# Kernel optimization log

Measured on AMD Instinct MI355X. Metric: run time of the kernel, lower is better.

Reference implementation:

```python
import jax, jax.numpy as jnp
import numpy as np

B, L, H, A = 512, 256, 512, 128
IENC, VDIM, EDIM, CDIM = 512, 512, 512, 512


def _lstm_cell(x, h, c, w_ih, w_hh, b_ih, b_hh):
    # PyTorch LSTMCell: gates ordered (i, f, g, o)
    gates = x @ w_ih.T + h @ w_hh.T + b_ih + b_hh
    i, f, g, o = jnp.split(gates, 4, axis=1)
    c_new = jax.nn.sigmoid(f) * c + jax.nn.sigmoid(i) * jnp.tanh(g)
    h_new = jax.nn.sigmoid(o) * jnp.tanh(c_new)
    return h_new, c_new


def setup_inputs() -> dict:
    key = jax.random.key(0)
    ks = jax.random.split(key, 32)
    s = 0.02  # param init scale
    d = {
        'xt': jax.random.normal(ks[0], (B, IENC), jnp.float32),
        'video': jax.random.normal(ks[1], (VDIM,), jnp.float32),
        'event': jax.random.normal(ks[2], (B, EDIM), jnp.float32),
        'clip': jax.random.normal(ks[3], (B, L, CDIM), jnp.float32),
        'clip_mask': jax.random.randint(ks[4], (B, L), 0, 2, jnp.int32),
        'state_h': jax.random.normal(ks[5], (3, B, H), jnp.float32),
        'state_c': jax.random.normal(ks[6], (3, B, H), jnp.float32),
        # layer0: in = VDIM + H + IENC
        'w_ih0': jax.random.normal(ks[7], (4 * H, VDIM + H + IENC), jnp.float32) * s,
        'w_hh0': jax.random.normal(ks[8], (4 * H, H), jnp.float32) * s,
        'b_ih0': jnp.zeros((4 * H,), jnp.float32),
        'b_hh0': jnp.zeros((4 * H,), jnp.float32),
        # layer1: in = EDIM + H
        'w_ih1': jax.random.normal(ks[9], (4 * H, EDIM + H), jnp.float32) * s,
        'w_hh1': jax.random.normal(ks[10], (4 * H, H), jnp.float32) * s,
        'b_ih1': jnp.zeros((4 * H,), jnp.float32),
        'b_hh1': jnp.zeros((4 * H,), jnp.float32),
        # layer2: in = CDIM + H
        'w_ih2': jax.random.normal(ks[11], (4 * H, CDIM + H), jnp.float32) * s,
        'w_hh2': jax.random.normal(ks[12], (4 * H, H), jnp.float32) * s,
        'b_ih2': jnp.zeros((4 * H,), jnp.float32),
        'b_hh2': jnp.zeros((4 * H,), jnp.float32),
        # attention params
        'wc': jax.random.normal(ks[13], (A, CDIM), jnp.float32) * s,
        'bc': jnp.zeros((A,), jnp.float32),
        'wh': jax.random.normal(ks[14], (A, H), jnp.float32) * s,
        'bh': jnp.zeros((A,), jnp.float32),
        'wa': jax.random.normal(ks[15], (1, A), jnp.float32) * s,
        'ba': jnp.zeros((1,), jnp.float32),
    }
    return d


def reference(xt, video, event, clip, clip_mask, state_h, state_c,
              w_ih0, w_hh0, b_ih0, b_hh0,
              w_ih1, w_hh1, b_ih1, b_hh1,
              w_ih2, w_hh2, b_ih2, b_hh2,
              wc, bc, wh, bh, wa, ba):
    pre_h = state_h[-1]                                   # [B,H]
    video_b = jnp.broadcast_to(video[None, :], (xt.shape[0], video.shape[0]))
    # layer 0 (dropout is identity in eval mode)
    x0 = jnp.concatenate([xt, video_b, pre_h], axis=1)
    h0, c0 = _lstm_cell(x0, state_h[0], state_c[0], w_ih0, w_hh0, b_ih0, b_hh0)
    # layer 1
    x1 = jnp.concatenate([event, h0], axis=1)
    h1, c1 = _lstm_cell(x1, state_h[1], state_c[1], w_ih1, w_hh1, b_ih1, b_hh1)
    # Bahdanau additive attention over clip tokens
    att = jnp.einsum('blc,ac->bla', clip, wc) + bc        # [B,L,A]
    att_h = h1 @ wh.T + bh                                # [B,A]
    dot = jnp.tanh(att + att_h[:, None, :])               # [B,L,A]
    scores = jnp.einsum('bla,a->bl', dot, wa[0]) + ba[0]  # [B,L]
    weight = jax.nn.softmax(scores, axis=1)
    m = clip_mask.astype(weight.dtype)
    weight = weight * m
    weight = weight / jnp.sum(weight, axis=1, keepdims=True)
    att_res = jnp.einsum('bl,blc->bc', weight, clip)      # [B,CDIM]
    # layer 2
    x2 = jnp.concatenate([att_res, h1], axis=1)
    h2, c2 = _lstm_cell(x2, state_h[2], state_c[2], w_ih2, w_hh2, b_ih2, b_hh2)
    new_h = jnp.stack([h0, h1, h2])
    new_c = jnp.stack([c0, c1, c2])
    return h2, new_h, new_c
```

## Files before the change

### kernel.cpp

```cpp
#include <hip/hip_runtime.h>
#include <math.h>

typedef __attribute__((ext_vector_type(8))) short bf16x8;
typedef __attribute__((ext_vector_type(4))) float f32x4;

constexpr int LST = 72;
constexpr int AST = 520;

__device__ __forceinline__ unsigned short f2b(float f) {
    union { float f; unsigned int i; } c; c.f = f;
    unsigned int i = c.i;
    return (unsigned short)((i + 0x7fffu + ((i >> 16) & 1u)) >> 16);
}
__device__ __forceinline__ void unpack2(unsigned int v, float& lo, float& hi) {
    union { unsigned int i; float f; } c0, c1;
    c0.i = v << 16; c1.i = v & 0xffff0000u;
    lo = c0.f; hi = c1.f;
}
__device__ __forceinline__ uint2 pack4(float4 v) {
    uint2 pk;
    pk.x = (unsigned int)f2b(v.x) | ((unsigned int)f2b(v.y) << 16);
    pk.y = (unsigned int)f2b(v.z) | ((unsigned int)f2b(v.w) << 16);
    return pk;
}
__device__ __forceinline__ float sigf(float x) { return 1.f / (1.f + __expf(-x)); }
__device__ __forceinline__ float tanhfast(float x) { return 1.f - 2.f / (1.f + __expf(2.f * x)); }

template<int NT>
__device__ __forceinline__ void gate_body(
    int bx, int t, unsigned short* Al, unsigned short* Bl,
    const float* __restrict__ A0, const float* __restrict__ A1,
    const float* __restrict__ A2, const float* __restrict__ A3,
    int as0, int as1, int as2, int as3,
    const float* __restrict__ B0, const float* __restrict__ B1,
    const float* __restrict__ B2, const float* __restrict__ B3,
    int bs0, int bs1, int bs2, int bs3,
    const float* __restrict__ b_ih, const float* __restrict__ b_hh,
    const float* __restrict__ c_prev, float* __restrict__ h_out,
    float* __restrict__ c_out, float* __restrict__ h_dup, int K)
{
    constexpr int BM = NT / 4;
    constexpr int MBLK = 512 / BM;
    constexpr int NA = BM * 16 / NT;
    constexpr int NB = 1024 / NT;
    const int mb = bx % MBLK, jb = bx / MBLK;
    const int m0 = mb * BM, j0 = jb * 16;
    const int w = t >> 6, lane = t & 63;
    const int col = lane & 15, hi = lane >> 4;

    f32x4 acc[4];
#pragma unroll
    for (int g = 0; g < 4; ++g)
#pragma unroll
        for (int r = 0; r < 4; ++r) acc[g][r] = 0.f;

    for (int kt = 0; kt < K; kt += 64) {
        const int p = kt >> 9, kin = kt & 511;
        const float* ap = (p == 0) ? A0 : (p == 1) ? A1 : (p == 2) ? A2 : A3;
        const int astr   = (p == 0) ? as0 : (p == 1) ? as1 : (p == 2) ? as2 : as3;
        const float* bp = (p == 0) ? B0 : (p == 1) ? B1 : (p == 2) ? B2 : B3;
        const int bstr   = (p == 0) ? bs0 : (p == 1) ? bs1 : (p == 2) ? bs2 : bs3;
        float4 ta[NA], tb[NB];
#pragma unroll
        for (int k = 0; k < NA; ++k) {
            const int c = t + k * NT, row = c >> 4, q = c & 15;
            ta[k] = *(const float4*)(ap + (astr ? (size_t)(m0 + row) * astr : 0) + kin + q * 4);
        }
#pragma unroll
        for (int k = 0; k < NB; ++k) {
            const int c = t + k * NT, row = c >> 4, q = c & 15;
            const int brow = (row >> 4) * 512 + j0 + (row & 15);
            tb[k] = *(const float4*)(bp + (size_t)brow * bstr + kin + q * 4);
        }
        __syncthreads();
#pragma unroll
        for (int k = 0; k < NA; ++k) {
            const int c = t + k * NT, row = c >> 4, q = c & 15;
            *(uint2*)&Al[row * LST + q * 4] = pack4(ta[k]);
        }
#pragma unroll
        for (int k = 0; k < NB; ++k) {
            const int c = t + k * NT, row = c >> 4, q = c & 15;
            *(uint2*)&Bl[row * LST + q * 4] = pack4(tb[k]);
        }
        __syncthreads();
#pragma unroll
        for (int sub = 0; sub < 2; ++sub) {
            const int ko = sub * 32 + hi * 8;
            const bf16x8 af = *(const bf16x8*)&Al[(w * 16 + col) * LST + ko];
#pragma unroll
            for (int g = 0; g < 4; ++g) {
                const bf16x8 bfr = *(const bf16x8*)&Bl[(g * 16 + col) * LST + ko];
                acc[g] = __builtin_amdgcn_mfma_f32_16x16x32_bf16(af, bfr, acc[g], 0, 0, 0);
            }
        }
    }
    const int j = j0 + col;
    const float bi = b_ih[j]        + b_hh[j];
    const float bf = b_ih[512 + j]  + b_hh[512 + j];
    const float bg = b_ih[1024 + j] + b_hh[1024 + j];
    const float bo = b_ih[1536 + j] + b_hh[1536 + j];
#pragma unroll
    for (int r = 0; r < 4; ++r) {
        const int bidx = m0 + w * 16 + hi * 4 + r;
        const size_t off = (size_t)bidx * 512 + j;
        const float gi = acc[0][r] + bi, gf = acc[1][r] + bf;
        const float gg = acc[2][r] + bg, go = acc[3][r] + bo;
        const float c = c_prev[off];
        const float cn = sigf(gf) * c + sigf(gi) * tanhfast(gg);
        const float hn = sigf(go) * tanhfast(cn);
        h_out[off] = hn;
        c_out[off] = cn;
        if (h_dup) h_dup[off] = hn;
    }
}

__device__ __forceinline__ void att1_body(
    int mb, int t, unsigned short* Ab, unsigned short* Bt, int* s_act,
    const float* __restrict__ clip, const float* __restrict__ wc,
    const float* __restrict__ bc, const int* __restrict__ mask,
    unsigned short* __restrict__ att)
{
    const int m0 = mb * 32;
    if (t < 32) s_act[t] = mask[m0 + t];
    __syncthreads();

#pragma unroll
    for (int h = 0; h < 2; ++h) {
        float4 tmp[8];
#pragma unroll
        for (int k = 0; k < 8; ++k) {
            const int c = t + ((h * 8 + k) << 8), row = c >> 7, q = c & 127;
            if (s_act[row]) tmp[k] = *(const float4*)(clip + (size_t)(m0 + row) * 512 + q * 4);
        }
#pragma unroll
        for (int k = 0; k < 8; ++k) {
            const int c = t + ((h * 8 + k) << 8), row = c >> 7, q = c & 127;
            if (s_act[row]) *(uint2*)&Ab[row * AST + q * 4] = pack4(tmp[k]);
        }
    }

    const int w = t >> 6, lane = t & 63;
    const int col = lane & 15, hi = lane >> 4;
    f32x4 acc[2][2];
#pragma unroll
    for (int i = 0; i < 2; ++i)
#pragma unroll
        for (int j = 0; j < 2; ++j)
#pragma unroll
            for (int r = 0; r < 4; ++r) acc[i][j][r] = 0.f;

    for (int kt = 0; kt < 8; ++kt) {
        const int k0 = kt * 64;
        float4 tb[8];
#pragma unroll
        for (int k = 0; k < 8; ++k) {
            const int c = t + (k << 8), row = c >> 4, q = c & 15;
            tb[k] = *(const float4*)(wc + (size_t)row * 512 + k0 + q * 4);
        }
        __syncthreads();
#pragma unroll
        for (int k = 0; k < 8; ++k) {
            const int c = t + (k << 8), row = c >> 4, q = c & 15;
            *(uint2*)&Bt[row * LST + q * 4] = pack4(tb[k]);
        }
        __syncthreads();
#pragma unroll
        for (int sub = 0; sub < 2; ++sub) {
            const int ko = sub * 32 + hi * 8;
            bf16x8 af[2], bfr[2];
            af[0] = *(const bf16x8*)&Ab[col * AST + k0 + ko];
            af[1] = *(const bf16x8*)&Ab[(16 + col) * AST + k0 + ko];
            bfr[0] = *(const bf16x8*)&Bt[(w * 32 + col) * LST + ko];
            bfr[1] = *(const bf16x8*)&Bt[(w * 32 + 16 + col) * LST + ko];
#pragma unroll
            for (int i = 0; i < 2; ++i)
#pragma unroll
                for (int j = 0; j < 2; ++j)
                    acc[i][j] = __builtin_amdgcn_mfma_f32_16x16x32_bf16(af[i], bfr[j], acc[i][j], 0, 0, 0);
        }
    }
#pragma unroll
    for (int i = 0; i < 2; ++i)
#pragma unroll
        for (int j = 0; j < 2; ++j) {
            const int n = w * 32 + j * 16 + col;
            const float bias = bc[n];
#pragma unroll
            for (int r = 0; r < 4; ++r) {
                const int m = i * 16 + hi * 4 + r;
                if (s_act[m])
                    att[(size_t)(m0 + m) * 128 + n] = f2b(acc[i][j][r] + bias);
            }
        }
}

__global__ __launch_bounds__(256, 3)
void k1_fused(const float* xt, const float* video, const float* sh2, const float* sh0,
              const float* w_ih0, const float* w_hh0, const float* b_ih0, const float* b_hh0,
              const float* c_prev0, float* h_out0, float* c_out0,
              const float* clip, const float* wc, const float* bc,
              const int* mask, unsigned short* att)
{
    __shared__ unsigned short Ab[32 * AST];
    __shared__ unsigned short Bt[128 * LST];
    __shared__ int s_act[32];
    if (blockIdx.x < 256) {
        gate_body<256>(blockIdx.x, threadIdx.x, Ab, Bt,
                       xt, video, sh2, sh0, 512, 0, 512, 512,
                       w_ih0, w_ih0 + 512, w_ih0 + 1024, w_hh0, 1536, 1536, 1536, 512,
                       b_ih0, b_hh0, c_prev0, h_out0, c_out0, nullptr, 2048);
    } else {
        att1_body(blockIdx.x - 256, threadIdx.x, Ab, Bt, s_act, clip, wc, bc, mask, att);
    }
}

__global__ __launch_bounds__(256, 3)
void k2_fused(const float* event, const float* h0, const float* sh1,
              const float* w_ih1, const float* w_hh1, const float* b_ih1, const float* b_hh1,
              const float* c_prev1, float* h_out1, float* c_out1,
              const float* clip, const float* wc, const float* bc,
              const int* mask, unsigned short* att)
{
    __shared__ unsigned short Ab[32 * AST];
    __shared__ unsigned short Bt[128 * LST];
    __shared__ int s_act[32];
    if (blockIdx.x < 256) {
        gate_body<256>(blockIdx.x, threadIdx.x, Ab, Bt,
                       event, h0, sh1, nullptr, 512, 512, 512, 0,
                       w_ih1, w_ih1 + 512, w_hh1, nullptr, 1024, 1024, 512, 0,
                       b_ih1, b_hh1, c_prev1, h_out1, c_out1, nullptr, 1536);
    } else {
        att1_body(3072 + (int)blockIdx.x - 256, threadIdx.x, Ab, Bt, s_act, clip, wc, bc, mask, att);
    }
}

__global__ __launch_bounds__(128, 4)
void gate_layer(const float* A0, const float* A1, const float* A2,
                int as0, int as1, int as2,
                const float* w_ih, const float* w_hh,
                const float* b_ih, const float* b_hh,
                const float* c_prev, float* h_out, float* c_out, float* h_dup, int K)
{
    __shared__ unsigned short Al[32 * LST];
    __shared__ unsigned short Bl[64 * LST];
    gate_body<128>(blockIdx.x, threadIdx.x, Al, Bl,
                   A0, A1, A2, nullptr, as0, as1, as2, 0,
                   w_ih, w_ih + 512, w_hh, nullptr, 1024, 1024, 512, 0,
                   b_ih, b_hh, c_prev, h_out, c_out, h_dup, K);
}

__global__ __launch_bounds__(256)
void att2_kernel(const unsigned short* __restrict__ att, const float* __restrict__ h1,
                 const float* __restrict__ wh, const float* __restrict__ bh,
                 const float* __restrict__ wa, const float* __restrict__ ba,
                 const float* __restrict__ clip, const int* __restrict__ mask,
                 float* __restrict__ att_res)
{
    __shared__ float s_h1[512];
    __shared__ float s_atth[128];
    __shared__ float s_part[256];
    __shared__ float s_wa[128];
    __shared__ float s_sc[256];
    __shared__ float s_red[8];
    __shared__ float s_w[256];
    __shared__ int s_idx[256];
    __shared__ int s_cnt;
    const int b = blockIdx.x, t = threadIdx.x;
    if (t == 0) s_cnt = 0;
    const int act = mask[(size_t)b * 256 + t];

    s_h1[t]       = h1[(size_t)b * 512 + t];
    s_h1[256 + t] = h1[(size_t)b * 512 + 256 + t];
    if (t < 128) s_wa[t] = wa[t];
    __syncthreads();

    {
        const int a = t & 127, half = t >> 7;
        const float4* wr4 = (const float4*)(wh + (size_t)a * 512 + half * 256);
        const float* hh = s_h1 + half * 256;
        float s = 0.f;
#pragma unroll 4
        for (int k4 = 0; k4 < 64; ++k4) {
            const float4 vv = wr4[k4];
            const float* hp = hh + k4 * 4;
            s += vv.x * hp[0] + vv.y * hp[1] + vv.z * hp[2] + vv.w * hp[3];
        }
        s_part[t] = s;
    }
    __syncthreads();
    if (t < 128) s_atth[t] = s_part[t] + s_part[128 + t] + bh[t];
    __syncthreads();

    {
        const uint4* ar4 = (const uint4*)(att + ((size_t)b * 256 + t) * 128);
        float s = ba[0];
#pragma unroll 4
        for (int k8 = 0; k8 < 16; ++k8) {
            const uint4 vv = ar4[k8];
            float v0, v1, v2, v3, v4, v5, v6, v7;
            unpack2(vv.x, v0, v1); unpack2(vv.y, v2, v3);
            unpack2(vv.z, v4, v5); unpack2(vv.w, v6, v7);
            const int a0 = k8 * 8;
            s += s_wa[a0 + 0] * tanhfast(v0 + s_atth[a0 + 0]);
            s += s_wa[a0 + 1] * tanhfast(v1 + s_atth[a0 + 1]);
            s += s_wa[a0 + 2] * tanhfast(v2 + s_atth[a0 + 2]);
            s += s_wa[a0 + 3] * tanhfast(v3 + s_atth[a0 + 3]);
            s += s_wa[a0 + 4] * tanhfast(v4 + s_atth[a0 + 4]);
            s += s_wa[a0 + 5] * tanhfast(v5 + s_atth[a0 + 5]);
            s += s_wa[a0 + 6] * tanhfast(v6 + s_atth[a0 + 6]);
            s += s_wa[a0 + 7] * tanhfast(v7 + s_atth[a0 + 7]);
        }
        s_sc[t] = s;
    }
    __syncthreads();

    float v = act ? s_sc[t] : -3.4e38f;
    for (int off = 32; off > 0; off >>= 1) v = fmaxf(v, __shfl_down(v, off));
    if ((t & 63) == 0) s_red[t >> 6] = v;
    __syncthreads();
    if (t == 0) s_red[4] = fmaxf(fmaxf(s_red[0], s_red[1]), fmaxf(s_red[2], s_red[3]));
    __syncthreads();
    const float mx = s_red[4];
    const float e = act ? __expf(s_sc[t] - mx) : 0.f;
    float sv = e;
    for (int off = 32; off > 0; off >>= 1) sv += __shfl_down(sv, off);
    if ((t & 63) == 0) s_red[t >> 6] = sv;
    __syncthreads();
    if (t == 0) s_red[5] = s_red[0] + s_red[1] + s_red[2] + s_red[3];
    __syncthreads();
    const float wgt = e / s_red[5];
    if (wgt != 0.f) {
        const int pos = atomicAdd(&s_cnt, 1);
        s_idx[pos] = t;
        s_w[pos] = wgt;
    }
    __syncthreads();
    const int cnt = s_cnt;

    float a0 = 0.f, a1 = 0.f;
    const float* cb = clip + (size_t)b * (256 * 512);
    int i = 0;
    for (; i + 8 <= cnt; i += 8) {
        float2 vv[8]; float ww[8];
#pragma unroll
        for (int u = 0; u < 8; ++u) {
            vv[u] = *(const float2*)&cb[s_idx[i + u] * 512 + 2 * t];
            ww[u] = s_w[i + u];
        }
#pragma unroll
        for (int u = 0; u < 8; ++u) { a0 += ww[u] * vv[u].x; a1 += ww[u] * vv[u].y; }
    }
    for (; i < cnt; ++i) {
        const float2 vv = *(const float2*)&cb[s_idx[i] * 512 + 2 * t];
        a0 += s_w[i] * vv.x;
        a1 += s_w[i] * vv.y;
    }
    float2 o; o.x = a0; o.y = a1;
    *(float2*)&att_res[(size_t)b * 512 + 2 * t] = o;
}

extern "C" void kernel_launch(void* const* d_in, const int* in_sizes, int n_in,
                              void* d_out, int out_size, void* d_ws, size_t ws_size,
                              hipStream_t stream) {
    typedef const float* cf;
    cf xt      = (cf)d_in[0];
    cf video   = (cf)d_in[1];
    cf event   = (cf)d_in[2];
    cf clip    = (cf)d_in[3];
    const int* mask = (const int*)d_in[4];
    cf state_h = (cf)d_in[5];
    cf state_c = (cf)d_in[6];
    cf w_ih0 = (cf)d_in[7],  w_hh0 = (cf)d_in[8],  b_ih0 = (cf)d_in[9],  b_hh0 = (cf)d_in[10];
    cf w_ih1 = (cf)d_in[11], w_hh1 = (cf)d_in[12], b_ih1 = (cf)d_in[13], b_hh1 = (cf)d_in[14];
    cf w_ih2 = (cf)d_in[15], w_hh2 = (cf)d_in[16], b_ih2 = (cf)d_in[17], b_hh2 = (cf)d_in[18];
    cf wc = (cf)d_in[19], bc = (cf)d_in[20];
    cf wh = (cf)d_in[21], bh = (cf)d_in[22];
    cf wa = (cf)d_in[23], ba = (cf)d_in[24];

    float* out = (float*)d_out;
    const int BH = 512 * 512;
    float* new_h = out + BH;
    float* new_c = out + 4 * BH;

    unsigned short* att = (unsigned short*)d_ws;
    float* att_res      = (float*)((char*)d_ws + (32u << 20));

    k1_fused<<<3328, 256, 0, stream>>>(
        xt, video, state_h + 2 * BH, state_h,
        w_ih0, w_hh0, b_ih0, b_hh0,
        state_c, new_h, new_c,
        clip, wc, bc, mask, att);

    k2_fused<<<1280, 256, 0, stream>>>(
        event, new_h, state_h + BH,
        w_ih1, w_hh1, b_ih1, b_hh1,
        state_c + BH, new_h + BH, new_c + BH,
        clip, wc, bc, mask, att);

    att2_kernel<<<512, 256, 0, stream>>>(att, new_h + BH, wh, bh, wa, ba, clip, mask, att_res);

    gate_layer<<<512, 128, 0, stream>>>(
        att_res, new_h + BH, state_h + 2 * BH, 512, 512, 512,
        w_ih2, w_hh2, b_ih2, b_hh2,
        state_c + 2 * BH, new_h + 2 * BH, new_c + 2 * BH, out, 1536);
}
```

Measured before the change: 665.0 us.

## Prepack weights and activations to bf16 in a separate pass before GEMMs

```diff
diff --git a/kernel.cpp b/kernel.cpp
--- a/kernel.cpp
+++ b/kernel.cpp
@@ -26,18 +26,53 @@
 __device__ __forceinline__ float sigf(float x) { return 1.f / (1.f + __expf(-x)); }
 __device__ __forceinline__ float tanhfast(float x) { return 1.f - 2.f / (1.f + __expf(2.f * x)); }
 
+__global__ __launch_bounds__(256)
+void prepack_kernel(const float* __restrict__ w_ih0, const float* __restrict__ w_hh0,
+                    const float* __restrict__ w_ih1, const float* __restrict__ w_hh1,
+                    const float* __restrict__ w_ih2, const float* __restrict__ w_hh2,
+                    const float* __restrict__ wc, const float* __restrict__ xt,
+                    const float* __restrict__ video, const float* __restrict__ state_h,
+                    const float* __restrict__ event, unsigned short* __restrict__ dst)
+{
+    const size_t NV = 11862528 / 8;
+    for (size_t g = (size_t)blockIdx.x * 256 + threadIdx.x; g < NV;
+         g += (size_t)gridDim.x * 256) {
+        const size_t e = g * 8;
+        const float* s; size_t o;
+        if      (e < 3145728)  { s = w_ih0;            o = e; }
+        else if (e < 4194304)  { s = w_hh0;            o = e - 3145728; }
+        else if (e < 6291456)  { s = w_ih1;            o = e - 4194304; }
+        else if (e < 7340032)  { s = w_hh1;            o = e - 6291456; }
+        else if (e < 9437184)  { s = w_ih2;            o = e - 7340032; }
+        else if (e < 10485760) { s = w_hh2;            o = e - 9437184; }
+        else if (e < 10551296) { s = wc;               o = e - 10485760; }
+        else if (e < 10813440) { s = xt;               o = e - 10551296; }
+        else if (e < 10813952) { s = video;            o = e - 10813440; }
+        else if (e < 11076096) { s = state_h;          o = e - 10813952; }
+        else if (e < 11338240) { s = state_h + 262144; o = e - 11076096; }
+        else if (e < 11600384) { s = state_h + 524288; o = e - 11338240; }
+        else                   { s = event;            o = e - 11600384; }
+        const float4 a = *(const float4*)(s + o);
+        const float4 b = *(const float4*)(s + o + 4);
+        const uint2 p0 = pack4(a), p1 = pack4(b);
+        uint4 ov; ov.x = p0.x; ov.y = p0.y; ov.z = p1.x; ov.w = p1.y;
+        *(uint4*)(dst + e) = ov;
+    }
+}
+
 template<int NT>
 __device__ __forceinline__ void gate_body(
     int bx, int t, unsigned short* Al, unsigned short* Bl,
-    const float* __restrict__ A0, const float* __restrict__ A1,
-    const float* __restrict__ A2, const float* __restrict__ A3,
+    const unsigned short* __restrict__ A0, const unsigned short* __restrict__ A1,
+    const unsigned short* __restrict__ A2, const unsigned short* __restrict__ A3,
     int as0, int as1, int as2, int as3,
-    const float* __restrict__ B0, const float* __restrict__ B1,
-    const float* __restrict__ B2, const float* __restrict__ B3,
+    const unsigned short* __restrict__ B0, const unsigned short* __restrict__ B1,
+    const unsigned short* __restrict__ B2, const unsigned short* __restrict__ B3,
     int bs0, int bs1, int bs2, int bs3,
     const float* __restrict__ b_ih, const float* __restrict__ b_hh,
     const float* __restrict__ c_prev, float* __restrict__ h_out,
-    float* __restrict__ c_out, float* __restrict__ h_dup, int K)
+    float* __restrict__ c_out, float* __restrict__ h_dup,
+    unsigned short* __restrict__ hb_out, int K)
 {
     constexpr int BM = NT / 4;
     constexpr int MBLK = 512 / BM;
@@ -56,32 +91,32 @@
 
     for (int kt = 0; kt < K; kt += 64) {
         const int p = kt >> 9, kin = kt & 511;
-        const float* ap = (p == 0) ? A0 : (p == 1) ? A1 : (p == 2) ? A2 : A3;
-        const int astr   = (p == 0) ? as0 : (p == 1) ? as1 : (p == 2) ? as2 : as3;
-        const float* bp = (p == 0) ? B0 : (p == 1) ? B1 : (p == 2) ? B2 : B3;
-        const int bstr   = (p == 0) ? bs0 : (p == 1) ? bs1 : (p == 2) ? bs2 : bs3;
-        float4 ta[NA], tb[NB];
+        const unsigned short* ap = (p == 0) ? A0 : (p == 1) ? A1 : (p == 2) ? A2 : A3;
+        const int astr           = (p == 0) ? as0 : (p == 1) ? as1 : (p == 2) ? as2 : as3;
+        const unsigned short* bp = (p == 0) ? B0 : (p == 1) ? B1 : (p == 2) ? B2 : B3;
+        const int bstr           = (p == 0) ? bs0 : (p == 1) ? bs1 : (p == 2) ? bs2 : bs3;
+        uint2 ta[NA], tb[NB];
 #pragma unroll
         for (int k = 0; k < NA; ++k) {
             const int c = t + k * NT, row = c >> 4, q = c & 15;
-            ta[k] = *(const float4*)(ap + (astr ? (size_t)(m0 + row) * astr : 0) + kin + q * 4);
+            ta[k] = *(const uint2*)(ap + (astr ? (size_t)(m0 + row) * astr : 0) + kin + q * 4);
         }
 #pragma unroll
         for (int k = 0; k < NB; ++k) {
             const int c = t + k * NT, row = c >> 4, q = c & 15;
             const int brow = (row >> 4) * 512 + j0 + (row & 15);
-            tb[k] = *(const float4*)(bp + (size_t)brow * bstr + kin + q * 4);
+            tb[k] = *(const uint2*)(bp + (size_t)brow * bstr + kin + q * 4);
         }
         __syncthreads();
 #pragma unroll
         for (int k = 0; k < NA; ++k) {
             const int c = t + k * NT, row = c >> 4, q = c & 15;
-            *(uint2*)&Al[row * LST + q * 4] = pack4(ta[k]);
+            *(uint2*)&Al[row * LST + q * 4] = ta[k];
         }
 #pragma unroll
         for (int k = 0; k < NB; ++k) {
             const int c = t + k * NT, row = c >> 4, q = c & 15;
-            *(uint2*)&Bl[row * LST + q * 4] = pack4(tb[k]);
+            *(uint2*)&Bl[row * LST + q * 4] = tb[k];
         }
         __syncthreads();
 #pragma unroll
@@ -112,12 +147,13 @@
         h_out[off] = hn;
         c_out[off] = cn;
         if (h_dup) h_dup[off] = hn;
+        if (hb_out) hb_out[off] = f2b(hn);
     }
 }
 
 __device__ __forceinline__ void att1_body(
     int mb, int t, unsigned short* Ab, unsigned short* Bt, int* s_act,
-    const float* __restrict__ clip, const float* __restrict__ wc,
+    const float* __restrict__ clip, const unsigned short* __restrict__ wcb,
     const float* __restrict__ bc, const int* __restrict__ mask,
     unsigned short* __restrict__ att)
 {
@@ -152,17 +188,17 @@
 
     for (int kt = 0; kt < 8; ++kt) {
         const int k0 = kt * 64;
-        float4 tb[8];
+        uint2 tb[8];
 #pragma unroll
         for (int k = 0; k < 8; ++k) {
             const int c = t + (k << 8), row = c >> 4, q = c & 15;
-            tb[k] = *(const float4*)(wc + (size_t)row * 512 + k0 + q * 4);
+            tb[k] = *(const uint2*)(wcb + (size_t)row * 512 + k0 + q * 4);
         }
         __syncthreads();
 #pragma unroll
         for (int k = 0; k < 8; ++k) {
             const int c = t + (k << 8), row = c >> 4, q = c & 15;
-            *(uint2*)&Bt[row * LST + q * 4] = pack4(tb[k]);
+            *(uint2*)&Bt[row * LST + q * 4] = tb[k];
         }
         __syncthreads();
 #pragma unroll
@@ -196,10 +232,12 @@
 }
 
 __global__ __launch_bounds__(256, 3)
-void k1_fused(const float* xt, const float* video, const float* sh2, const float* sh0,
-              const float* w_ih0, const float* w_hh0, const float* b_ih0, const float* b_hh0,
-              const float* c_prev0, float* h_out0, float* c_out0,
-              const float* clip, const float* wc, const float* bc,
+void k1_fused(const unsigned short* xtb, const unsigned short* videob,
+              const unsigned short* sh2b, const unsigned short* sh0b,
+              const unsigned short* wb0, const unsigned short* wbh0,
+              const float* b_ih0, const float* b_hh0,
+              const float* c_prev0, float* h_out0, float* c_out0, unsigned short* h0b,
+              const float* clip, const unsigned short* wcb, const float* bc,
               const int* mask, unsigned short* att)
 {
     __shared__ unsigned short Ab[32 * AST];
@@ -207,19 +245,20 @@
     __shared__ int s_act[32];
     if (blockIdx.x < 256) {
         gate_body<256>(blockIdx.x, threadIdx.x, Ab, Bt,
-                       xt, video, sh2, sh0, 512, 0, 512, 512,
-                       w_ih0, w_ih0 + 512, w_ih0 + 1024, w_hh0, 1536, 1536, 1536, 512,
-                       b_ih0, b_hh0, c_prev0, h_out0, c_out0, nullptr, 2048);
+                       xtb, videob, sh2b, sh0b, 512, 0, 512, 512,
+                       wb0, wb0 + 512, wb0 + 1024, wbh0, 1536, 1536, 1536, 512,
+                       b_ih0, b_hh0, c_prev0, h_out0, c_out0, nullptr, h0b, 2048);
     } else {
-        att1_body(blockIdx.x - 256, threadIdx.x, Ab, Bt, s_act, clip, wc, bc, mask, att);
+        att1_body(blockIdx.x - 256, threadIdx.x, Ab, Bt, s_act, clip, wcb, bc, mask, att);
     }
 }
 
 __global__ __launch_bounds__(256, 3)
-void k2_fused(const float* event, const float* h0, const float* sh1,
-              const float* w_ih1, const float* w_hh1, const float* b_ih1, const float* b_hh1,
-              const float* c_prev1, float* h_out1, float* c_out1,
-              const float* clip, const float* wc, const float* bc,
+void k2_fused(const unsigned short* evb, const unsigned short* h0b, const unsigned short* sh1b,
+              const unsigned short* wb1, const unsigned short* wbh1,
+              const float* b_ih1, const float* b_hh1,
+              const float* c_prev1, float* h_out1, float* c_out1, unsigned short* h1b,
+              const float* clip, const unsigned short* wcb, const float* bc,
               const int* mask, unsigned short* att)
 {
     __shared__ unsigned short Ab[32 * AST];
@@ -227,18 +266,18 @@
     __shared__ int s_act[32];
     if (blockIdx.x < 256) {
         gate_body<256>(blockIdx.x, threadIdx.x, Ab, Bt,
-                       event, h0, sh1, nullptr, 512, 512, 512, 0,
-                       w_ih1, w_ih1 + 512, w_hh1, nullptr, 1024, 1024, 512, 0,
-                       b_ih1, b_hh1, c_prev1, h_out1, c_out1, nullptr, 1536);
+                       evb, h0b, sh1b, nullptr, 512, 512, 512, 0,
+                       wb1, wb1 + 512, wbh1, nullptr, 1024, 1024, 512, 0,
+                       b_ih1, b_hh1, c_prev1, h_out1, c_out1, nullptr, h1b, 1536);
     } else {
-        att1_body(3072 + (int)blockIdx.x - 256, threadIdx.x, Ab, Bt, s_act, clip, wc, bc, mask, att);
+        att1_body(3072 + (int)blockIdx.x - 256, threadIdx.x, Ab, Bt, s_act, clip, wcb, bc, mask, att);
     }
 }
 
 __global__ __launch_bounds__(128, 4)
-void gate_layer(const float* A0, const float* A1, const float* A2,
+void gate_layer(const unsigned short* A0, const unsigned short* A1, const unsigned short* A2,
                 int as0, int as1, int as2,
-                const float* w_ih, const float* w_hh,
+                const unsigned short* wb, const unsigned short* wbh,
                 const float* b_ih, const float* b_hh,
                 const float* c_prev, float* h_out, float* c_out, float* h_dup, int K)
 {
@@ -246,8 +285,8 @@
     __shared__ unsigned short Bl[64 * LST];
     gate_body<128>(blockIdx.x, threadIdx.x, Al, Bl,
                    A0, A1, A2, nullptr, as0, as1, as2, 0,
-                   w_ih, w_ih + 512, w_hh, nullptr, 1024, 1024, 512, 0,
-                   b_ih, b_hh, c_prev, h_out, c_out, h_dup, K);
+                   wb, wb + 512, wbh, nullptr, 1024, 1024, 512, 0,
+                   b_ih, b_hh, c_prev, h_out, c_out, h_dup, nullptr, K);
 }
 
 __global__ __launch_bounds__(256)
@@ -255,7 +294,7 @@
                  const float* __restrict__ wh, const float* __restrict__ bh,
                  const float* __restrict__ wa, const float* __restrict__ ba,
                  const float* __restrict__ clip, const int* __restrict__ mask,
-                 float* __restrict__ att_res)
+                 unsigned short* __restrict__ att_res_b)
 {
     __shared__ float s_h1[512];
     __shared__ float s_atth[128];
@@ -356,8 +395,8 @@
         a0 += s_w[i] * vv.x;
         a1 += s_w[i] * vv.y;
     }
-    float2 o; o.x = a0; o.y = a1;
-    *(float2*)&att_res[(size_t)b * 512 + 2 * t] = o;
+    const unsigned int ov = (unsigned int)f2b(a0) | ((unsigned int)f2b(a1) << 16);
+    *(unsigned int*)&att_res_b[(size_t)b * 512 + 2 * t] = ov;
 }
 
 extern "C" void kernel_launch(void* const* d_in, const int* in_sizes, int n_in,
@@ -384,24 +423,44 @@
     float* new_c = out + 4 * BH;
 
     unsigned short* att = (unsigned short*)d_ws;
-    float* att_res      = (float*)((char*)d_ws + (32u << 20));
+    unsigned short* pp  = (unsigned short*)((char*)d_ws + (32u << 20));
+    unsigned short* wb0    = pp + 0;
+    unsigned short* wbh0   = pp + 3145728;
+    unsigned short* wb1    = pp + 4194304;
+    unsigned short* wbh1   = pp + 6291456;
+    unsigned short* wb2    = pp + 7340032;
+    unsigned short* wbh2   = pp + 9437184;
+    unsigned short* wcb    = pp + 10485760;
+    unsigned short* xtb    = pp + 10551296;
+    unsigned short* videob = pp + 10813440;
+    unsigned short* sh0b   = pp + 10813952;
+    unsigned short* sh1b   = pp + 11076096;
+    unsigned short* sh2b   = pp + 11338240;
+    unsigned short* evb    = pp + 11600384;
+    unsigned short* h0b    = pp + 11862528;
+    unsigned short* h1b    = pp + 12124672;
+    unsigned short* arb    = pp + 12386816;
+
+    prepack_kernel<<<2048, 256, 0, stream>>>(
+        w_ih0, w_hh0, w_ih1, w_hh1, w_ih2, w_hh2, wc,
+        xt, video, state_h, event, pp);
 
     k1_fused<<<3328, 256, 0, stream>>>(
-        xt, video, state_h + 2 * BH, state_h,
-        w_ih0, w_hh0, b_ih0, b_hh0,
-        state_c, new_h, new_c,
-        clip, wc, bc, mask, att);
+        xtb, videob, sh2b, sh0b,
+        wb0, wbh0, b_ih0, b_hh0,
+        state_c, new_h, new_c, h0b,
+        clip, wcb, bc, mask, att);
 
     k2_fused<<<1280, 256, 0, stream>>>(
-        event, new_h, state_h + BH,
-        w_ih1, w_hh1, b_ih1, b_hh1,
-        state_c + BH, new_h + BH, new_c + BH,
-        clip, wc, bc, mask, att);
-
-    att2_kernel<<<512, 256, 0, stream>>>(att, new_h + BH, wh, bh, wa, ba, clip, mask, att_res);
+        evb, h0b, sh1b,
+        wb1, wbh1, b_ih1, b_hh1,
+        state_c + BH, new_h + BH, new_c + BH, h1b,
+        clip, wcb, bc, mask, att);
+
+    att2_kernel<<<512, 256, 0, stream>>>(att, new_h + BH, wh, bh, wa, ba, clip, mask, arb);
 
     gate_layer<<<512, 128, 0, stream>>>(
-        att_res, new_h + BH, state_h + 2 * BH, 512, 512, 512,
-        w_ih2, w_hh2, b_ih2, b_hh2,
+        arb, h1b, sh2b, 512, 512, 512,
+        wb2, wbh2, b_ih2, b_hh2,
         state_c + 2 * BH, new_h + 2 * BH, new_c + 2 * BH, out, 1536);
 }
```

After: 567.7 us. 14.6% less time.
